# Performance work log

Measured on AMD Instinct MI355X. Metric: run time of the kernel, lower is better.

## Reference

```python
import jax, jax.numpy as jnp
import numpy as np

TEMPERATURE = 0.1

def _l2norm(x):
    # F.normalize(dim=1) with eps clamp
    n = jnp.maximum(jnp.linalg.norm(x, axis=1, keepdims=True), 1e-12)
    return x / n

def _retrieval_metric(s):
    # T=1: position of the diagonal element in each row's descending sort.
    order = jnp.argsort(-s, axis=1)            # [N,N] descending argsort
    rankpos = jnp.argsort(order, axis=1)        # inverse permutation: rank of each column
    pos = jnp.diagonal(rankpos)                 # j such that rank[i][j] == i
    posf = pos.astype(s.dtype)
    r1 = jnp.mean((pos < 1).astype(s.dtype))
    r5 = jnp.mean((pos < 5).astype(s.dtype))
    r10 = jnp.mean((pos < 10).astype(s.dtype))
    mr = jnp.mean(posf)
    return r1, r5, r10, mr

def setup_inputs() -> dict:
    key = jax.random.key(0)
    k1, k2, k3, k4 = jax.random.split(key, 4)
    N, C = 4096, 512
    return {
        'v_feat': jax.random.normal(k1, (N, C), dtype=jnp.float32),
        't_feat': jax.random.normal(k2, (N, C), dtype=jnp.float32),
        'p_v': jax.random.normal(k3, (N, C), dtype=jnp.float32),
        'p_t': jax.random.normal(k4, (N, C), dtype=jnp.float32),
    }

def reference(v_feat, t_feat, p_v, p_t):
    vn = _l2norm(v_feat)
    tn = _l2norm(t_feat)
    pvn = _l2norm(p_v)
    ptn = _l2norm(p_t)
    sv = jnp.einsum('nc,mc->nm', vn, ptn) / TEMPERATURE  # [N,N]
    st = jnp.einsum('nc,mc->nm', tn, pvn) / TEMPERATURE  # [N,N]
    # nominator: scalar logsumexp over both diagonals (2N values)
    nominator = jax.nn.logsumexp(jnp.concatenate([jnp.diagonal(sv), jnp.diagonal(st)], axis=0))
    # denominator: per-row logsumexp over concatenated [N,2N]
    denominator = jax.nn.logsumexp(jnp.concatenate([sv, st], axis=1), axis=1)
    loss = jnp.mean(denominator - nominator)
    # metrics (no-grad path in original)
    v_std = jnp.mean(jnp.std(vn, axis=0, ddof=1))
    t_std = jnp.mean(jnp.std(tn, axis=0, ddof=1))
    pv_std = jnp.mean(jnp.std(pvn, axis=0, ddof=1))
    pt_std = jnp.mean(jnp.std(ptn, axis=0, ddof=1))
    sv_raw = jnp.einsum('nc,mc->nm', vn, ptn)
    st_raw = jnp.einsum('nc,mc->nm', tn, pvn)
    v_r1, v_r5, v_r10, v_mr = _retrieval_metric(sv_raw)
    t_r1, t_r5, t_r10, t_mr = _retrieval_metric(st_raw)
    return (loss, v_std, t_std, pv_std, pt_std,
            v_r1, v_r5, v_r10, v_mr,
            t_r1, t_r5, t_r10, t_mr)
```

## Files before the change

kernel.cpp:

```cpp
#include <hip/hip_runtime.h>
#include <hip/hip_bf16.h>

#define N 4096
#define C 512

typedef __attribute__((ext_vector_type(8))) short bf16x8;
typedef __attribute__((ext_vector_type(8))) short s16x8;
typedef __attribute__((ext_vector_type(4))) float f32x4;

__device__ inline float bf2f(__hip_bfloat16 h) { return __bfloat162float(h); }
__device__ inline float bfbits2f(unsigned short b) {
    union { unsigned u; float f; } c; c.u = ((unsigned)b) << 16; return c.f;
}

__device__ inline void gload16(const void* g, void* l) {
    __builtin_amdgcn_global_load_lds(
        (__attribute__((address_space(1))) void*)(g),
        (__attribute__((address_space(3))) void*)(l),
        16, 0, 0);
}

__global__ __launch_bounds__(256) void k_norm_split(
    const float* __restrict__ s0, const float* __restrict__ s1f,
    const float* __restrict__ s2f, const float* __restrict__ s3,
    __hip_bfloat16* __restrict__ ws_hi0, long mat_stride)
{
    const int m = blockIdx.x >> 12;
    const int row = blockIdx.x & 4095;
    const int tid = threadIdx.x;
    const float* src = (m == 0) ? s0 : (m == 1) ? s1f : (m == 2) ? s2f : s3;
    __hip_bfloat16* hi = ws_hi0 + (long)m * mat_stride;
    __hip_bfloat16* lo = hi + (long)N * C;

    const float2* r = (const float2*)(src + (size_t)row * C);
    float2 x = r[tid];
    float ss = x.x * x.x + x.y * x.y;
    for (int o = 1; o < 64; o <<= 1) ss += __shfl_xor(ss, o);
    __shared__ float wsum[4];
    if ((tid & 63) == 0) wsum[tid >> 6] = ss;
    __syncthreads();
    float tot = wsum[0] + wsum[1] + wsum[2] + wsum[3];
    float scale = 1.0f / fmaxf(sqrtf(tot), 1e-12f);
    float y0 = x.x * scale, y1 = x.y * scale;
    __hip_bfloat16 h0 = __float2bfloat16(y0);
    __hip_bfloat16 h1 = __float2bfloat16(y1);
    __hip_bfloat16 l0 = __float2bfloat16(y0 - bf2f(h0));
    __hip_bfloat16 l1 = __float2bfloat16(y1 - bf2f(h1));
    size_t base = (size_t)row * C + 2 * tid;
    hi[base] = h0; hi[base + 1] = h1;
    lo[base] = l0; lo[base + 1] = l1;
}

__global__ __launch_bounds__(256) void k_diag(
    const unsigned short* __restrict__ h0, const unsigned short* __restrict__ l0,
    const unsigned short* __restrict__ h1, const unsigned short* __restrict__ l1,
    const unsigned short* __restrict__ h2, const unsigned short* __restrict__ l2,
    const unsigned short* __restrict__ h3, const unsigned short* __restrict__ l3,
    float* __restrict__ dv, float* __restrict__ dt)
{
    const int lane = threadIdx.x & 63;
    const int w = threadIdx.x >> 6;
    const int row = blockIdx.x * 4 + w;
    const int z = blockIdx.y;
    const unsigned short* ah = z ? h1 : h0;
    const unsigned short* al = z ? l1 : l0;
    const unsigned short* bh = z ? h2 : h3;
    const unsigned short* bl = z ? l2 : l3;
    float* dout = z ? dt : dv;

    size_t base = (size_t)row * C + lane * 8;
    s16x8 xh = *(const s16x8*)(ah + base);
    s16x8 xl = *(const s16x8*)(al + base);
    s16x8 yh = *(const s16x8*)(bh + base);
    s16x8 yl = *(const s16x8*)(bl + base);
    float s = 0.f;
    for (int e = 0; e < 8; e++) {
        float a = bfbits2f((unsigned short)xh[e]);
        float b = bfbits2f((unsigned short)xl[e]);
        float c = bfbits2f((unsigned short)yh[e]);
        float d = bfbits2f((unsigned short)yl[e]);
        s += a * c + a * d + b * c;
    }
    for (int o = 1; o < 64; o <<= 1) s += __shfl_xor(s, o);
    if (lane == 0) dout[row] = s;
}

__global__ __launch_bounds__(256) void k_gemm(
    const __hip_bfloat16* __restrict__ h0, const __hip_bfloat16* __restrict__ l0,
    const __hip_bfloat16* __restrict__ h1, const __hip_bfloat16* __restrict__ l1,
    const __hip_bfloat16* __restrict__ h2, const __hip_bfloat16* __restrict__ l2,
    const __hip_bfloat16* __restrict__ h3, const __hip_bfloat16* __restrict__ l3,
    const float* __restrict__ dv, const float* __restrict__ dt,
    float* __restrict__ pev, float* __restrict__ pet,
    float* __restrict__ pcv, float* __restrict__ pct)
{
    __shared__ __align__(16) __hip_bfloat16 sA[2][128][32];
    __shared__ __align__(16) __hip_bfloat16 sB[2][128][32];
    __shared__ float sdiag[128];
    __shared__ float sred[128][2][2];

    const int z = blockIdx.z;
    const __hip_bfloat16* Ah = z ? h1 : h0;
    const __hip_bfloat16* Al = z ? l1 : l0;
    const __hip_bfloat16* Bh = z ? h2 : h3;
    const __hip_bfloat16* Bl = z ? l2 : l3;
    const float* diag = z ? dt : dv;
    float* pe = z ? pet : pev;
    float* pc = z ? pct : pcv;

    const int tid = threadIdx.x;
    const int lane = tid & 63;
    const int w = tid >> 6;
    const int wy = w >> 1, wx = w & 1;
    const int bm = blockIdx.x * 128;
    const int bn = blockIdx.y * 128;

    if (tid < 128) sdiag[tid] = diag[bm + tid];

    f32x4 acc[4][4];
    for (int i = 0; i < 4; i++)
        for (int j = 0; j < 4; j++)
            acc[i][j] = (f32x4){0.f, 0.f, 0.f, 0.f};

    const int srow = lane >> 2;
    const int scol = (lane & 3) * 8;
    const int fr = lane & 15;
    const int fq = (lane >> 4) * 8;

    for (int k0 = 0; k0 < C; k0 += 32) {
        for (int half = 0; half < 2; half++) {
            int rr = w * 16 + half * 64 + srow;
            size_t ga = (size_t)(bm + rr) * C + k0 + scol;
            size_t gb = (size_t)(bn + rr) * C + k0 + scol;
            gload16(Ah + ga, &sA[0][rr][scol]);
            gload16(Al + ga, &sA[1][rr][scol]);
            gload16(Bh + gb, &sB[0][rr][scol]);
            gload16(Bl + gb, &sB[1][rr][scol]);
        }
        __syncthreads();

        bf16x8 a_h[4], a_l[4], b_h[4], b_l[4];
        for (int i = 0; i < 4; i++) {
            a_h[i] = *(const bf16x8*)&sA[0][wy * 64 + i * 16 + fr][fq];
            a_l[i] = *(const bf16x8*)&sA[1][wy * 64 + i * 16 + fr][fq];
            b_h[i] = *(const bf16x8*)&sB[0][wx * 64 + i * 16 + fr][fq];
            b_l[i] = *(const bf16x8*)&sB[1][wx * 64 + i * 16 + fr][fq];
        }
        for (int i = 0; i < 4; i++)
            for (int j = 0; j < 4; j++) {
                acc[i][j] = __builtin_amdgcn_mfma_f32_16x16x32_bf16(a_h[i], b_h[j], acc[i][j], 0, 0, 0);
                acc[i][j] = __builtin_amdgcn_mfma_f32_16x16x32_bf16(a_h[i], b_l[j], acc[i][j], 0, 0, 0);
                acc[i][j] = __builtin_amdgcn_mfma_f32_16x16x32_bf16(a_l[i], b_h[j], acc[i][j], 0, 0, 0);
            }
        __syncthreads();
    }

    const int quad = lane >> 4;
    for (int i = 0; i < 4; i++) {
        for (int reg = 0; reg < 4; reg++) {
            int rloc = wy * 64 + i * 16 + quad * 4 + reg;
            int grow = bm + rloc;
            float d = sdiag[rloc];
            float e = 0.f, c = 0.f;
            for (int j = 0; j < 4; j++) {
                float s = acc[i][j][reg];
                int gcol = bn + wx * 64 + j * 16 + fr;
                e += __expf(10.f * s - 10.f);
                if (s > d && gcol != grow) c += 1.f;
            }
            for (int o = 1; o < 16; o <<= 1) {
                e += __shfl_xor(e, o);
                c += __shfl_xor(c, o);
            }
            if (fr == 0) { sred[rloc][wx][0] = e; sred[rloc][wx][1] = c; }
        }
    }
    __syncthreads();
    if (tid < 128) {
        size_t idx = (size_t)(bm + tid) * 32 + blockIdx.y;
        pe[idx] = sred[tid][0][0] + sred[tid][1][0];
        pc[idx] = sred[tid][0][1] + sred[tid][1][1];
    }
}

__global__ __launch_bounds__(512) void k_stdp(
    const __hip_bfloat16* __restrict__ ws_hi0, long mat_stride,
    float* __restrict__ s1, float* __restrict__ s2)
{
    const int col = threadIdx.x;
    const int chunk = blockIdx.x;
    const int m = blockIdx.y;
    const __hip_bfloat16* hi = ws_hi0 + (long)m * mat_stride;
    const __hip_bfloat16* lo = hi + (long)N * C;
    float a = 0.f, b = 0.f;
    for (int r = chunk * 64; r < chunk * 64 + 64; r++) {
        float y = bf2f(hi[(size_t)r * C + col]) + bf2f(lo[(size_t)r * C + col]);
        a += y;
        b += y * y;
    }
    size_t idx = ((size_t)m * 64 + chunk) * 512 + col;
    s1[idx] = a;
    s2[idx] = b;
}

__global__ __launch_bounds__(64) void k_rowred(
    const float* __restrict__ dv, const float* __restrict__ dt,
    const float* __restrict__ pev, const float* __restrict__ pet,
    const float* __restrict__ pcv, const float* __restrict__ pct,
    float* __restrict__ partials)
{
    const int lane = threadIdx.x;
    const int row = blockIdx.x * 64 + lane;

    float se = 0.f, pv = 0.f, pt = 0.f;
    for (int cb = 0; cb < 32; cb++) {
        se += pev[(size_t)row * 32 + cb] + pet[(size_t)row * 32 + cb];
        pv += pcv[(size_t)row * 32 + cb];
        pt += pct[(size_t)row * 32 + cb];
    }

    float vals[10];
    vals[0] = logf(se) + 10.f;
    vals[1] = (pv < 0.5f) ? 1.f : 0.f;
    vals[2] = (pv < 4.5f) ? 1.f : 0.f;
    vals[3] = (pv < 9.5f) ? 1.f : 0.f;
    vals[4] = pv;
    vals[5] = (pt < 0.5f) ? 1.f : 0.f;
    vals[6] = (pt < 4.5f) ? 1.f : 0.f;
    vals[7] = (pt < 9.5f) ? 1.f : 0.f;
    vals[8] = pt;
    vals[9] = __expf(10.f * dv[row] - 10.f) + __expf(10.f * dt[row] - 10.f);

    for (int k = 0; k < 10; k++) {
        float v = vals[k];
        for (int o = 1; o < 64; o <<= 1) v += __shfl_xor(v, o);
        if (lane == k) partials[(size_t)blockIdx.x * 10 + k] = v;
    }
}

__global__ __launch_bounds__(64) void k_colstd(
    const float* __restrict__ s1, const float* __restrict__ s2,
    float* __restrict__ stdpart)
{
    const int lane = threadIdx.x;
    const int m = blockIdx.x >> 3;
    const int col = (blockIdx.x & 7) * 64 + lane;
    float a = 0.f, b = 0.f;
    for (int ch = 0; ch < 64; ch++) {
        size_t idx = ((size_t)m * 64 + ch) * 512 + col;
        a += s1[idx];
        b += s2[idx];
    }
    float var = (b - a * a * (1.f / N)) * (1.f / (N - 1));
    float sd = sqrtf(fmaxf(var, 0.f));
    for (int o = 1; o < 64; o <<= 1) sd += __shfl_xor(sd, o);
    if (lane == 0) stdpart[blockIdx.x] = sd;
}

__global__ __launch_bounds__(64) void k_final2(
    const float* __restrict__ partials,
    const float* __restrict__ stdpart,
    float* __restrict__ out)
{
    const int lane = threadIdx.x;
    float v = 0.f;
    if (lane < 10) {
        for (int b = 0; b < 64; b++) v += partials[b * 10 + lane];
    }
    __shared__ float g[10];
    __shared__ float stds[4];
    if (lane < 10) g[lane] = v;
    if (lane < 4) {
        float s = 0.f;
        for (int i = 0; i < 8; i++) s += stdpart[lane * 8 + i];
        stds[lane] = s * (1.f / 512.f);
    }
    __syncthreads();
    if (lane == 0) {
        const float invN = 1.f / N;
        float nominator = logf(g[9]) + 10.f;
        out[0]  = g[0] * invN - nominator;
        out[1]  = stds[0];
        out[2]  = stds[1];
        out[3]  = stds[2];
        out[4]  = stds[3];
        out[5]  = g[1] * invN;
        out[6]  = g[2] * invN;
        out[7]  = g[3] * invN;
        out[8]  = g[4] * invN;
        out[9]  = g[5] * invN;
        out[10] = g[6] * invN;
        out[11] = g[7] * invN;
        out[12] = g[8] * invN;
    }
}

extern "C" void kernel_launch(void* const* d_in, const int* in_sizes, int n_in,
                              void* d_out, int out_size, void* d_ws, size_t ws_size,
                              hipStream_t stream)
{
    char* p = (char*)d_ws;
    const size_t NE = (size_t)N * C;
    const long mat_stride = 2 * NE;
    __hip_bfloat16* hiA[4];
    __hip_bfloat16* loA[4];
    for (int m = 0; m < 4; m++) {
        hiA[m] = (__hip_bfloat16*)p; p += NE * 2;
        loA[m] = (__hip_bfloat16*)p; p += NE * 2;
    }
    float* dv  = (float*)p; p += N * 4;
    float* dt  = (float*)p; p += N * 4;
    float* pev = (float*)p; p += 32 * N * 4;
    float* pet = (float*)p; p += 32 * N * 4;
    float* pcv = (float*)p; p += 32 * N * 4;
    float* pct = (float*)p; p += 32 * N * 4;
    float* s1  = (float*)p; p += 4 * 64 * 512 * 4;
    float* s2  = (float*)p; p += 4 * 64 * 512 * 4;
    float* partials = (float*)p; p += 64 * 10 * 4;
    float* stdpart  = (float*)p; p += 32 * 4;

    k_norm_split<<<dim3(4 * N), 256, 0, stream>>>(
        (const float*)d_in[0], (const float*)d_in[1],
        (const float*)d_in[2], (const float*)d_in[3],
        hiA[0], mat_stride);

    k_diag<<<dim3(N / 4, 2), 256, 0, stream>>>(
        (const unsigned short*)hiA[0], (const unsigned short*)loA[0],
        (const unsigned short*)hiA[1], (const unsigned short*)loA[1],
        (const unsigned short*)hiA[2], (const unsigned short*)loA[2],
        (const unsigned short*)hiA[3], (const unsigned short*)loA[3],
        dv, dt);

    k_gemm<<<dim3(32, 32, 2), 256, 0, stream>>>(
        hiA[0], loA[0], hiA[1], loA[1], hiA[2], loA[2], hiA[3], loA[3],
        dv, dt, pev, pet, pcv, pct);

    k_stdp<<<dim3(64, 4), 512, 0, stream>>>(hiA[0], mat_stride, s1, s2);

    k_rowred<<<dim3(64), 64, 0, stream>>>(dv, dt, pev, pet, pcv, pct, partials);
    k_colstd<<<dim3(32), 64, 0, stream>>>(s1, s2, stdpart);
    k_final2<<<dim3(1), 64, 0, stream>>>(partials, stdpart, (float*)d_out);
}
```

Baseline: 223.5 us.

## Switch GEMM to 32x32 MFMA and vectorize normalize, std and row-reduce kernels

The split-bf16 GEMM moves from 16x16x32 MFMA tiles to 32x32x16 MFMA tiles with a matching epilogue row/column mapping. The aim is fewer LDS fragment reads and instructions per FLOP. The normalize kernel now handles one row per wavefront with float4 loads and 16-byte stores, with no shared-memory reduction. The column-std partial kernel and row reduction also use vectorized loads, and the std partial count drops from 64 to 32 chunks. The epilogue's 32-lane shuffle reduction and the changed accumulator layout carry some risk of mapping errors.

```diff
diff --git a/kernel.cpp b/kernel.cpp
--- a/kernel.cpp
+++ b/kernel.cpp
@@ -7,6 +7,7 @@
 typedef __attribute__((ext_vector_type(8))) short bf16x8;
 typedef __attribute__((ext_vector_type(8))) short s16x8;
 typedef __attribute__((ext_vector_type(4))) float f32x4;
+typedef __attribute__((ext_vector_type(16))) float f32x16;
 
 __device__ inline float bf2f(__hip_bfloat16 h) { return __bfloat162float(h); }
 __device__ inline float bfbits2f(unsigned short b) {
@@ -25,30 +26,33 @@
     const float* __restrict__ s2f, const float* __restrict__ s3,
     __hip_bfloat16* __restrict__ ws_hi0, long mat_stride)
 {
-    const int m = blockIdx.x >> 12;
-    const int row = blockIdx.x & 4095;
-    const int tid = threadIdx.x;
+    const int lane = threadIdx.x & 63;
+    const int w = threadIdx.x >> 6;
+    const int grow = blockIdx.x * 4 + w;
+    const int m = grow >> 12;
+    const int row = grow & 4095;
     const float* src = (m == 0) ? s0 : (m == 1) ? s1f : (m == 2) ? s2f : s3;
     __hip_bfloat16* hi = ws_hi0 + (long)m * mat_stride;
     __hip_bfloat16* lo = hi + (long)N * C;
 
-    const float2* r = (const float2*)(src + (size_t)row * C);
-    float2 x = r[tid];
-    float ss = x.x * x.x + x.y * x.y;
+    const float4* r4 = (const float4*)(src + (size_t)row * C);
+    float4 x0 = r4[lane * 2];
+    float4 x1 = r4[lane * 2 + 1];
+    float ss = x0.x*x0.x + x0.y*x0.y + x0.z*x0.z + x0.w*x0.w
+             + x1.x*x1.x + x1.y*x1.y + x1.z*x1.z + x1.w*x1.w;
     for (int o = 1; o < 64; o <<= 1) ss += __shfl_xor(ss, o);
-    __shared__ float wsum[4];
-    if ((tid & 63) == 0) wsum[tid >> 6] = ss;
-    __syncthreads();
-    float tot = wsum[0] + wsum[1] + wsum[2] + wsum[3];
-    float scale = 1.0f / fmaxf(sqrtf(tot), 1e-12f);
-    float y0 = x.x * scale, y1 = x.y * scale;
-    __hip_bfloat16 h0 = __float2bfloat16(y0);
-    __hip_bfloat16 h1 = __float2bfloat16(y1);
-    __hip_bfloat16 l0 = __float2bfloat16(y0 - bf2f(h0));
-    __hip_bfloat16 l1 = __float2bfloat16(y1 - bf2f(h1));
-    size_t base = (size_t)row * C + 2 * tid;
-    hi[base] = h0; hi[base + 1] = h1;
-    lo[base] = l0; lo[base + 1] = l1;
+    float scale = 1.0f / fmaxf(sqrtf(ss), 1e-12f);
+
+    float y[8] = { x0.x*scale, x0.y*scale, x0.z*scale, x0.w*scale,
+                   x1.x*scale, x1.y*scale, x1.z*scale, x1.w*scale };
+    __hip_bfloat16 hv[8], lv[8];
+    for (int e = 0; e < 8; e++) {
+        hv[e] = __float2bfloat16(y[e]);
+        lv[e] = __float2bfloat16(y[e] - bf2f(hv[e]));
+    }
+    size_t base = (size_t)row * C + lane * 8;
+    *(s16x8*)(hi + base) = *(s16x8*)hv;
+    *(s16x8*)(lo + base) = *(s16x8*)lv;
 }
 
 __global__ __launch_bounds__(256) void k_diag(
@@ -117,15 +121,15 @@
 
     if (tid < 128) sdiag[tid] = diag[bm + tid];
 
-    f32x4 acc[4][4];
-    for (int i = 0; i < 4; i++)
-        for (int j = 0; j < 4; j++)
-            acc[i][j] = (f32x4){0.f, 0.f, 0.f, 0.f};
+    f32x16 acc[2][2];
+    for (int i = 0; i < 2; i++)
+        for (int j = 0; j < 2; j++)
+            for (int e = 0; e < 16; e++) acc[i][j][e] = 0.f;
 
     const int srow = lane >> 2;
     const int scol = (lane & 3) * 8;
-    const int fr = lane & 15;
-    const int fq = (lane >> 4) * 8;
+    const int mrow = lane & 31;
+    const int khalf = (lane >> 5) * 8;
 
     for (int k0 = 0; k0 < C; k0 += 32) {
         for (int half = 0; half < 2; half++) {
@@ -139,40 +143,47 @@
         }
         __syncthreads();
 
-        bf16x8 a_h[4], a_l[4], b_h[4], b_l[4];
-        for (int i = 0; i < 4; i++) {
-            a_h[i] = *(const bf16x8*)&sA[0][wy * 64 + i * 16 + fr][fq];
-            a_l[i] = *(const bf16x8*)&sA[1][wy * 64 + i * 16 + fr][fq];
-            b_h[i] = *(const bf16x8*)&sB[0][wx * 64 + i * 16 + fr][fq];
-            b_l[i] = *(const bf16x8*)&sB[1][wx * 64 + i * 16 + fr][fq];
+        for (int ks = 0; ks < 2; ks++) {
+            const int kk = ks * 16 + khalf;
+            bf16x8 a_h[2], a_l[2], b_h[2], b_l[2];
+            for (int i = 0; i < 2; i++) {
+                a_h[i] = *(const bf16x8*)&sA[0][wy * 64 + i * 32 + mrow][kk];
+                a_l[i] = *(const bf16x8*)&sA[1][wy * 64 + i * 32 + mrow][kk];
+                b_h[i] = *(const bf16x8*)&sB[0][wx * 64 + i * 32 + mrow][kk];
+                b_l[i] = *(const bf16x8*)&sB[1][wx * 64 + i * 32 + mrow][kk];
+            }
+            for (int i = 0; i < 2; i++)
+                for (int j = 0; j < 2; j++)
+                    acc[i][j] = __builtin_amdgcn_mfma_f32_32x32x16_bf16(a_h[i], b_h[j], acc[i][j], 0, 0, 0);
+            for (int i = 0; i < 2; i++)
+                for (int j = 0; j < 2; j++)
+                    acc[i][j] = __builtin_amdgcn_mfma_f32_32x32x16_bf16(a_h[i], b_l[j], acc[i][j], 0, 0, 0);
+            for (int i = 0; i < 2; i++)
+                for (int j = 0; j < 2; j++)
+                    acc[i][j] = __builtin_amdgcn_mfma_f32_32x32x16_bf16(a_l[i], b_h[j], acc[i][j], 0, 0, 0);
         }
-        for (int i = 0; i < 4; i++)
-            for (int j = 0; j < 4; j++) {
-                acc[i][j] = __builtin_amdgcn_mfma_f32_16x16x32_bf16(a_h[i], b_h[j], acc[i][j], 0, 0, 0);
-                acc[i][j] = __builtin_amdgcn_mfma_f32_16x16x32_bf16(a_h[i], b_l[j], acc[i][j], 0, 0, 0);
-                acc[i][j] = __builtin_amdgcn_mfma_f32_16x16x32_bf16(a_l[i], b_h[j], acc[i][j], 0, 0, 0);
-            }
         __syncthreads();
     }
 
-    const int quad = lane >> 4;
-    for (int i = 0; i < 4; i++) {
-        for (int reg = 0; reg < 4; reg++) {
-            int rloc = wy * 64 + i * 16 + quad * 4 + reg;
+    const int colr = lane & 31;
+    const int halfg = lane >> 5;
+    for (int i = 0; i < 2; i++) {
+        for (int reg = 0; reg < 16; reg++) {
+            int rloc = wy * 64 + i * 32 + (reg & 3) + 8 * (reg >> 2) + 4 * halfg;
             int grow = bm + rloc;
             float d = sdiag[rloc];
             float e = 0.f, c = 0.f;
-            for (int j = 0; j < 4; j++) {
+            for (int j = 0; j < 2; j++) {
                 float s = acc[i][j][reg];
-                int gcol = bn + wx * 64 + j * 16 + fr;
+                int gcol = bn + wx * 64 + j * 32 + colr;
                 e += __expf(10.f * s - 10.f);
                 if (s > d && gcol != grow) c += 1.f;
             }
-            for (int o = 1; o < 16; o <<= 1) {
+            for (int o = 1; o < 32; o <<= 1) {
                 e += __shfl_xor(e, o);
                 c += __shfl_xor(c, o);
             }
-            if (fr == 0) { sred[rloc][wx][0] = e; sred[rloc][wx][1] = c; }
+            if (colr == 0) { sred[rloc][wx][0] = e; sred[rloc][wx][1] = c; }
         }
     }
     __syncthreads();
@@ -183,24 +194,45 @@
     }
 }
 
-__global__ __launch_bounds__(512) void k_stdp(
+__global__ __launch_bounds__(256) void k_stdp(
     const __hip_bfloat16* __restrict__ ws_hi0, long mat_stride,
     float* __restrict__ s1, float* __restrict__ s2)
 {
-    const int col = threadIdx.x;
+    const int t = threadIdx.x;
+    const int colg = t & 63;
+    const int slice = t >> 6;
     const int chunk = blockIdx.x;
     const int m = blockIdx.y;
-    const __hip_bfloat16* hi = ws_hi0 + (long)m * mat_stride;
-    const __hip_bfloat16* lo = hi + (long)N * C;
-    float a = 0.f, b = 0.f;
-    for (int r = chunk * 64; r < chunk * 64 + 64; r++) {
-        float y = bf2f(hi[(size_t)r * C + col]) + bf2f(lo[(size_t)r * C + col]);
-        a += y;
-        b += y * y;
-    }
-    size_t idx = ((size_t)m * 64 + chunk) * 512 + col;
-    s1[idx] = a;
-    s2[idx] = b;
+    const unsigned short* hi = (const unsigned short*)(ws_hi0 + (long)m * mat_stride);
+    const unsigned short* lo = hi + (size_t)N * C;
+
+    float a[8], b[8];
+    for (int e = 0; e < 8; e++) { a[e] = 0.f; b[e] = 0.f; }
+    const int row0 = chunk * 128 + slice * 32;
+    for (int r = 0; r < 32; r++) {
+        size_t addr = (size_t)(row0 + r) * C + colg * 8;
+        s16x8 h8 = *(const s16x8*)(hi + addr);
+        s16x8 l8 = *(const s16x8*)(lo + addr);
+        for (int e = 0; e < 8; e++) {
+            float y = bfbits2f((unsigned short)h8[e]) + bfbits2f((unsigned short)l8[e]);
+            a[e] += y;
+            b[e] += y * y;
+        }
+    }
+    __shared__ float sa[4][512];
+    __shared__ float sb[4][512];
+    for (int e = 0; e < 8; e++) {
+        sa[slice][colg * 8 + e] = a[e];
+        sb[slice][colg * 8 + e] = b[e];
+    }
+    __syncthreads();
+    for (int c = t; c < 512; c += 256) {
+        float A = sa[0][c] + sa[1][c] + sa[2][c] + sa[3][c];
+        float B = sb[0][c] + sb[1][c] + sb[2][c] + sb[3][c];
+        size_t idx = ((size_t)m * 32 + chunk) * 512 + c;
+        s1[idx] = A;
+        s2[idx] = B;
+    }
 }
 
 __global__ __launch_bounds__(64) void k_rowred(
@@ -213,10 +245,15 @@
     const int row = blockIdx.x * 64 + lane;
 
     float se = 0.f, pv = 0.f, pt = 0.f;
-    for (int cb = 0; cb < 32; cb++) {
-        se += pev[(size_t)row * 32 + cb] + pet[(size_t)row * 32 + cb];
-        pv += pcv[(size_t)row * 32 + cb];
-        pt += pct[(size_t)row * 32 + cb];
+    const float4* e4v = (const float4*)(pev + (size_t)row * 32);
+    const float4* e4t = (const float4*)(pet + (size_t)row * 32);
+    const float4* c4v = (const float4*)(pcv + (size_t)row * 32);
+    const float4* c4t = (const float4*)(pct + (size_t)row * 32);
+    for (int q = 0; q < 8; q++) {
+        float4 a = e4v[q], b = e4t[q], c = c4v[q], d = c4t[q];
+        se += a.x + a.y + a.z + a.w + b.x + b.y + b.z + b.w;
+        pv += c.x + c.y + c.z + c.w;
+        pt += d.x + d.y + d.z + d.w;
     }
 
     float vals[10];
@@ -246,8 +283,8 @@
     const int m = blockIdx.x >> 3;
     const int col = (blockIdx.x & 7) * 64 + lane;
     float a = 0.f, b = 0.f;
-    for (int ch = 0; ch < 64; ch++) {
-        size_t idx = ((size_t)m * 64 + ch) * 512 + col;
+    for (int ch = 0; ch < 32; ch++) {
+        size_t idx = ((size_t)m * 32 + ch) * 512 + col;
         a += s1[idx];
         b += s2[idx];
     }
@@ -314,12 +351,12 @@
     float* pet = (float*)p; p += 32 * N * 4;
     float* pcv = (float*)p; p += 32 * N * 4;
     float* pct = (float*)p; p += 32 * N * 4;
-    float* s1  = (float*)p; p += 4 * 64 * 512 * 4;
-    float* s2  = (float*)p; p += 4 * 64 * 512 * 4;
+    float* s1  = (float*)p; p += 4 * 32 * 512 * 4;
+    float* s2  = (float*)p; p += 4 * 32 * 512 * 4;
     float* partials = (float*)p; p += 64 * 10 * 4;
     float* stdpart  = (float*)p; p += 32 * 4;
 
-    k_norm_split<<<dim3(4 * N), 256, 0, stream>>>(
+    k_norm_split<<<dim3(4 * N / 4), 256, 0, stream>>>(
         (const float*)d_in[0], (const float*)d_in[1],
         (const float*)d_in[2], (const float*)d_in[3],
         hiA[0], mat_stride);
@@ -335,7 +372,7 @@
         hiA[0], loA[0], hiA[1], loA[1], hiA[2], loA[2], hiA[3], loA[3],
         dv, dt, pev, pet, pcv, pct);
 
-    k_stdp<<<dim3(64, 4), 512, 0, stream>>>(hiA[0], mat_stride, s1, s2);
+    k_stdp<<<dim3(32, 4), 256, 0, stream>>>(hiA[0], mat_stride, s1, s2);
 
     k_rowred<<<dim3(64), 64, 0, stream>>>(dv, dt, pev, pet, pcv, pct, partials);
     k_colstd<<<dim3(32), 64, 0, stream>>>(s1, s2, stdpart);
```

New measurement: 251.0 us. 12.3% more time.
